# Kernel optimization log

Hardware: AMD Instinct MI355X
Metric: run time of the kernel (lower is better)

## Reference

```python
import jax, jax.numpy as jnp
import numpy as np

N = 50000
E = 400000
IN_DIM = 256
HID = 64
HEADS = 8
OUT_DIM = 40
NEG_SLOPE = 0.2  # PyG GATConv leaky-relu slope


def gat_conv(x, src, dst, W, a_src, a_dst, bias, concat):
    """One PyG-style GATConv (eval mode, self-loops already appended).
    x: [N, in], W: [in, H*C], a_src/a_dst: [H, C], bias: [H*C] or [C]."""
    H, C = a_src.shape
    h = (x @ W).reshape(N, H, C)                       # [N, H, C]
    # per-node attention logits, gathered per edge
    e_src = (h * a_src[None]).sum(-1)                  # [N, H]
    e_dst = (h * a_dst[None]).sum(-1)                  # [N, H]
    alpha = jax.nn.leaky_relu(e_src[src] + e_dst[dst], NEG_SLOPE)  # [Etot, H]
    # segment softmax over incoming edges of each dst node
    amax = jax.ops.segment_max(alpha, dst, num_segments=N)         # [N, H]
    ex = jnp.exp(alpha - amax[dst])
    denom = jax.ops.segment_sum(ex, dst, num_segments=N)           # [N, H]
    coef = ex / denom[dst]                                         # [Etot, H]
    # weighted scatter-add of neighbor features
    msg = h[src] * coef[:, :, None]                                # [Etot, H, C]
    out = jax.ops.segment_sum(msg, dst, num_segments=N)            # [N, H, C]
    out = out.reshape(N, H * C) if concat else out.mean(axis=1)
    return out + bias


def setup_inputs() -> dict:
    key = jax.random.key(0)
    ks = jax.random.split(key, 10)
    x = jax.random.normal(ks[0], (N, IN_DIM), dtype=jnp.float32)
    edge_index = jax.random.randint(ks[1], (2, E), 0, N, dtype=jnp.int32)
    g1 = 1.0 / np.sqrt(IN_DIM)
    g2 = 1.0 / np.sqrt(HID * HEADS)
    W1 = jax.random.normal(ks[2], (IN_DIM, HEADS * HID), dtype=jnp.float32) * g1
    a_src1 = jax.random.normal(ks[3], (HEADS, HID), dtype=jnp.float32) * 0.1
    a_dst1 = jax.random.normal(ks[4], (HEADS, HID), dtype=jnp.float32) * 0.1
    b1 = jnp.zeros((HEADS * HID,), dtype=jnp.float32)
    W2 = jax.random.normal(ks[5], (HEADS * HID, OUT_DIM), dtype=jnp.float32) * g2
    a_src2 = jax.random.normal(ks[6], (1, OUT_DIM), dtype=jnp.float32) * 0.1
    a_dst2 = jax.random.normal(ks[7], (1, OUT_DIM), dtype=jnp.float32) * 0.1
    b2 = jnp.zeros((OUT_DIM,), dtype=jnp.float32)
    return {"x": x, "edge_index": edge_index, "W1": W1, "a_src1": a_src1,
            "a_dst1": a_dst1, "b1": b1, "W2": W2, "a_src2": a_src2,
            "a_dst2": a_dst2, "b2": b2}


def reference(x, edge_index, W1, a_src1, a_dst1, b1, W2, a_src2, a_dst2, b2):
    # append self loops (PyG GATConv default add_self_loops=True)
    loop = jnp.arange(N, dtype=edge_index.dtype)
    src = jnp.concatenate([edge_index[0], loop])
    dst = jnp.concatenate([edge_index[1], loop])
    h = gat_conv(x, src, dst, W1, a_src1, a_dst1, b1, concat=True)
    h = jax.nn.elu(h)
    # dropout is identity in eval mode
    out = gat_conv(h, src, dst, W2, a_src2, a_dst2, b2, concat=False)
    return out
```

## Files before the change

kernel.cpp:

```cpp
#include <hip/hip_runtime.h>
#include <hip/hip_bf16.h>
#include <math.h>

#define IN_DIM 256
#define HEADS 8
#define HID 64
#define HC1 512
#define OUT_DIM 40
#define NEG_SLOPE 0.2f
#define CAP 64

typedef __attribute__((ext_vector_type(8))) short short8;
typedef __attribute__((ext_vector_type(4))) float f32x4;

__device__ __forceinline__ unsigned short f2b(float f) {
    __hip_bfloat16 h = __float2bfloat16(f);
    unsigned short u;
    __builtin_memcpy(&u, &h, 2);
    return u;
}

#define LRELU(a) ((a) > 0.f ? (a) : NEG_SLOPE * (a))

#define NB_W ((HC1 * IN_DIM + 48 * HC1 + 255) / 256)

__global__ __launch_bounds__(256) void prologue_kernel(
    const float* __restrict__ W1, const float* __restrict__ W2,
    __hip_bfloat16* __restrict__ W1T, __hip_bfloat16* __restrict__ W2T,
    const int* __restrict__ ei, int* __restrict__ cnt,
    int* __restrict__ csr_src, int E, int ET)
{
    int b = blockIdx.x;
    if (b < NB_W) {
        int i = b * 256 + threadIdx.x;
        if (i < HC1 * IN_DIM) {
            int n = i >> 8, k = i & 255;
            W1T[i] = __float2bfloat16(W1[(size_t)k * HC1 + n]);
        }
        int j = i - HC1 * IN_DIM;
        if (j >= 0 && j < 48 * HC1) {
            int n = j >> 9, k = j & 511;
            W2T[j] = __float2bfloat16(n < OUT_DIM ? W2[(size_t)k * OUT_DIM + n] : 0.f);
        }
    } else {
        int e = (b - NB_W) * 256 + threadIdx.x;
        if (e >= ET) return;
        int s, d;
        if (e < E) { s = ei[e]; d = ei[E + e]; } else { s = d = e - E; }
        int pos = atomicAdd(&cnt[d], 1);
        csr_src[((size_t)d << 6) + pos] = s;
    }
}

__global__ __launch_bounds__(512) void gemm1_mfma(
    const float* __restrict__ x, const __hip_bfloat16* __restrict__ W1T,
    const float* __restrict__ a_src1, const float* __restrict__ a_dst1,
    __hip_bfloat16* __restrict__ h1, float* __restrict__ e_src1,
    float* __restrict__ e_dst1, int N)
{
    __shared__ __hip_bfloat16 As[64][268];
    const int tid = threadIdx.x;
    const int row0 = blockIdx.x * 64;

    {
        int rr = tid >> 3;
        int cb = (tid & 7) * 32;
        int rowc = row0 + rr; if (rowc >= N) rowc = N - 1;
        const float* xp = x + (size_t)rowc * IN_DIM + cb;
#pragma unroll
        for (int j = 0; j < 4; ++j) {
            float4 a0 = *(const float4*)(xp + 8 * j);
            float4 a1 = *(const float4*)(xp + 8 * j + 4);
            short8 v;
            v[0] = f2b(a0.x); v[1] = f2b(a0.y); v[2] = f2b(a0.z); v[3] = f2b(a0.w);
            v[4] = f2b(a1.x); v[5] = f2b(a1.y); v[6] = f2b(a1.z); v[7] = f2b(a1.w);
            *(short8*)(&As[rr][cb + 8 * j]) = v;
        }
    }
    __syncthreads();

    const int w = tid >> 6;
    const int lane = tid & 63;
    const int r = lane & 15, g = lane >> 4;

    f32x4 acc[4][4] = {};
    const short* bp = (const short*)W1T + (size_t)(w * 64 + r) * IN_DIM + 8 * g;

#pragma unroll 2
    for (int kk = 0; kk < IN_DIM; kk += 32) {
        short8 af[4];
#pragma unroll
        for (int rt = 0; rt < 4; ++rt)
            af[rt] = *(const short8*)(&As[rt * 16 + r][kk + 8 * g]);
        short8 bf[4];
#pragma unroll
        for (int t = 0; t < 4; ++t)
            bf[t] = *(const short8*)(bp + (size_t)t * 16 * IN_DIM + kk);
#pragma unroll
        for (int t = 0; t < 4; ++t)
#pragma unroll
            for (int rt = 0; rt < 4; ++rt)
                acc[rt][t] = __builtin_amdgcn_mfma_f32_16x16x32_bf16(
                    af[rt], bf[t], acc[rt][t], 0, 0, 0);
    }

#pragma unroll
    for (int rt = 0; rt < 4; ++rt)
#pragma unroll
        for (int t = 0; t < 4; ++t) {
            int c = w * 64 + t * 16 + r;
#pragma unroll
            for (int q = 0; q < 4; ++q) {
                int row = row0 + rt * 16 + 4 * g + q;
                if (row < N)
                    h1[(size_t)row * HC1 + c] = __float2bfloat16(acc[rt][t][q]);
            }
        }

    float a1v[4], a2v[4];
#pragma unroll
    for (int t = 0; t < 4; ++t) {
        a1v[t] = a_src1[w * 64 + t * 16 + r];
        a2v[t] = a_dst1[w * 64 + t * 16 + r];
    }
#pragma unroll
    for (int rt = 0; rt < 4; ++rt) {
        float ps[4] = {}, pd[4] = {};
#pragma unroll
        for (int t = 0; t < 4; ++t)
#pragma unroll
            for (int q = 0; q < 4; ++q) {
                ps[q] += acc[rt][t][q] * a1v[t];
                pd[q] += acc[rt][t][q] * a2v[t];
            }
#pragma unroll
        for (int off = 1; off < 16; off <<= 1)
#pragma unroll
            for (int q = 0; q < 4; ++q) {
                ps[q] += __shfl_xor(ps[q], off);
                pd[q] += __shfl_xor(pd[q], off);
            }
        if (r == 0) {
#pragma unroll
            for (int q = 0; q < 4; ++q) {
                int row = row0 + rt * 16 + 4 * g + q;
                if (row < N) {
                    e_src1[row * 8 + w] = ps[q];
                    e_dst1[row * 8 + w] = pd[q];
                }
            }
        }
    }
}

__global__ __launch_bounds__(256) void gather1_kernel(
    const int* __restrict__ cnt, const int* __restrict__ csr_src,
    const __hip_bfloat16* __restrict__ h1, const float* __restrict__ e_src,
    const float* __restrict__ e_dst, const float* __restrict__ b1,
    __hip_bfloat16* __restrict__ hmid, int N)
{
    int d = blockIdx.x * 4 + (threadIdx.x >> 6);
    if (d >= N) return;
    const int lane = threadIdx.x & 63;
    const int h0 = lane >> 3;
    const size_t base = (size_t)d << 6;
    const int deg = cnt[d];
    const float edv = e_dst[d * 8 + (lane & 7)];

    float acc[8] = {};
    float ssum = 0.f;

    const int nch = (deg + 7) >> 3;
    for (int c = 0; c < nch; ++c) {
        int i = c * 8 + (lane >> 3);
        int ii = i < deg ? i : deg - 1;
        int s = csr_src[base + ii];
        float v = e_src[s * 8 + (lane & 7)] + edv;
        float coef = (i < deg) ? __expf(LRELU(v)) : 0.f;

        int emax = deg - c * 8; if (emax > 8) emax = 8;
        for (int e = 0; e < emax; ++e) {
            float ce = __shfl(coef, e * 8 + h0);
            int se = __shfl(s, e * 8);
            uint4 u = *(const uint4*)(h1 + ((size_t)se << 9) + 8 * lane);
            acc[0] += ce * __uint_as_float(u.x << 16);
            acc[1] += ce * __uint_as_float(u.x & 0xffff0000u);
            acc[2] += ce * __uint_as_float(u.y << 16);
            acc[3] += ce * __uint_as_float(u.y & 0xffff0000u);
            acc[4] += ce * __uint_as_float(u.z << 16);
            acc[5] += ce * __uint_as_float(u.z & 0xffff0000u);
            acc[6] += ce * __uint_as_float(u.w << 16);
            acc[7] += ce * __uint_as_float(u.w & 0xffff0000u);
            ssum += ce;
        }
    }

    float inv = 1.f / ssum;
    float4 b0 = *(const float4*)(b1 + 8 * lane);
    float4 b4 = *(const float4*)(b1 + 8 * lane + 4);
    float ob[8];
    ob[0] = acc[0] * inv + b0.x; ob[1] = acc[1] * inv + b0.y;
    ob[2] = acc[2] * inv + b0.z; ob[3] = acc[3] * inv + b0.w;
    ob[4] = acc[4] * inv + b4.x; ob[5] = acc[5] * inv + b4.y;
    ob[6] = acc[6] * inv + b4.z; ob[7] = acc[7] * inv + b4.w;
    unsigned short rr[8];
#pragma unroll
    for (int j = 0; j < 8; ++j) {
        float o = ob[j];
        o = o > 0.f ? o : expm1f(o);
        rr[j] = f2b(o);
    }
    *(uint4*)(hmid + (size_t)d * HC1 + 8 * lane) = *(uint4*)rr;
}

__global__ __launch_bounds__(256) void gemm2_mfma(
    const __hip_bfloat16* __restrict__ hmid, const __hip_bfloat16* __restrict__ W2T,
    const float* __restrict__ a_src2, const float* __restrict__ a_dst2,
    __hip_bfloat16* __restrict__ h2, float* __restrict__ e_src2,
    float* __restrict__ e_dst2, int N)
{
    __shared__ __hip_bfloat16 Bs[48][520];
    const int tid = threadIdx.x;

    {
        const short* wp = (const short*)W2T;
#pragma unroll
        for (int i = 0; i < 12; ++i) {
            int idx = tid + i * 256;
            int row = idx >> 6, ch = idx & 63;
            *(short8*)(&Bs[row][ch * 8]) = *(const short8*)(wp + (size_t)row * HC1 + ch * 8);
        }
    }
    __syncthreads();

    const int w = tid >> 6;
    const int lane = tid & 63;
    const int r = lane & 15, g = lane >> 4;
    const int rowW = blockIdx.x * 64 + w * 16;

    int arow = rowW + r; if (arow >= N) arow = N - 1;
    const short* ap = (const short*)hmid + (size_t)arow * HC1 + 8 * g;

    f32x4 acc[3] = {};
#pragma unroll 4
    for (int kk = 0; kk < HC1; kk += 32) {
        short8 af = *(const short8*)(ap + kk);
        short8 bf[3];
#pragma unroll
        for (int t = 0; t < 3; ++t)
            bf[t] = *(const short8*)(&Bs[t * 16 + r][kk + 8 * g]);
#pragma unroll
        for (int t = 0; t < 3; ++t)
            acc[t] = __builtin_amdgcn_mfma_f32_16x16x32_bf16(af, bf[t], acc[t], 0, 0, 0);
    }

#pragma unroll
    for (int t = 0; t < 3; ++t) {
        int c = t * 16 + r;
        if (c < OUT_DIM) {
#pragma unroll
            for (int q = 0; q < 4; ++q) {
                int row = rowW + 4 * g + q;
                if (row < N) h2[(size_t)row * OUT_DIM + c] = __float2bfloat16(acc[t][q]);
            }
        }
    }

    float as[3], ad[3];
#pragma unroll
    for (int t = 0; t < 3; ++t) {
        int c = t * 16 + r;
        as[t] = (c < OUT_DIM) ? a_src2[c] : 0.f;
        ad[t] = (c < OUT_DIM) ? a_dst2[c] : 0.f;
    }
    float ps[4] = {}, pd[4] = {};
#pragma unroll
    for (int t = 0; t < 3; ++t)
#pragma unroll
        for (int q = 0; q < 4; ++q) {
            ps[q] += acc[t][q] * as[t];
            pd[q] += acc[t][q] * ad[t];
        }
#pragma unroll
    for (int off = 1; off < 16; off <<= 1)
#pragma unroll
        for (int q = 0; q < 4; ++q) {
            ps[q] += __shfl_xor(ps[q], off);
            pd[q] += __shfl_xor(pd[q], off);
        }
    if (r == 0) {
#pragma unroll
        for (int q = 0; q < 4; ++q) {
            int row = rowW + 4 * g + q;
            if (row < N) { e_src2[row] = ps[q]; e_dst2[row] = pd[q]; }
        }
    }
}

__global__ __launch_bounds__(256) void gather2_kernel(
    const int* __restrict__ cnt, const int* __restrict__ csr_src,
    const __hip_bfloat16* __restrict__ h2, const float* __restrict__ e_src,
    const float* __restrict__ e_dst, const float* __restrict__ b2,
    float* __restrict__ out, int N)
{
    int wid = (blockIdx.x * blockDim.x + threadIdx.x) >> 6;
    if (wid >= N) return;
    int lane = threadIdx.x & 63;
    const size_t base = (size_t)wid << 6;
    const int end = cnt[wid];
    float ed = e_dst[wid];
    bool act = lane < OUT_DIM;
    int ln = act ? lane : 0;
    const unsigned short* h2u = (const unsigned short*)h2;

    float acc = 0.f, ssum = 0.f;
    int j = 0;
    for (; j + 4 <= end; j += 4) {
        int s0 = csr_src[base + j], s1 = csr_src[base + j + 1];
        int s2 = csr_src[base + j + 2], s3 = csr_src[base + j + 3];
        float v0 = e_src[s0] + ed, v1 = e_src[s1] + ed;
        float v2 = e_src[s2] + ed, v3 = e_src[s3] + ed;
        unsigned f0 = h2u[(size_t)s0 * OUT_DIM + ln];
        unsigned f1 = h2u[(size_t)s1 * OUT_DIM + ln];
        unsigned f2 = h2u[(size_t)s2 * OUT_DIM + ln];
        unsigned f3 = h2u[(size_t)s3 * OUT_DIM + ln];
        float e0 = __expf(LRELU(v0)), e1 = __expf(LRELU(v1));
        float e2 = __expf(LRELU(v2)), e3 = __expf(LRELU(v3));
        acc += e0 * __uint_as_float(f0 << 16) + e1 * __uint_as_float(f1 << 16)
             + e2 * __uint_as_float(f2 << 16) + e3 * __uint_as_float(f3 << 16);
        ssum += e0 + e1 + e2 + e3;
    }
    for (; j < end; ++j) {
        int s0 = csr_src[base + j];
        float v0 = e_src[s0] + ed;
        unsigned f0 = h2u[(size_t)s0 * OUT_DIM + ln];
        float e0 = __expf(LRELU(v0));
        acc += e0 * __uint_as_float(f0 << 16);
        ssum += e0;
    }
    if (act)
        out[(size_t)wid * OUT_DIM + lane] = acc / ssum + b2[lane];
}

extern "C" void kernel_launch(void* const* d_in, const int* in_sizes, int n_in,
                              void* d_out, int out_size, void* d_ws, size_t ws_size,
                              hipStream_t stream)
{
    const float* x      = (const float*)d_in[0];
    const int*   ei     = (const int*)d_in[1];
    const float* W1     = (const float*)d_in[2];
    const float* a_src1 = (const float*)d_in[3];
    const float* a_dst1 = (const float*)d_in[4];
    const float* b1     = (const float*)d_in[5];
    const float* W2     = (const float*)d_in[6];
    const float* a_src2 = (const float*)d_in[7];
    const float* a_dst2 = (const float*)d_in[8];
    const float* b2     = (const float*)d_in[9];
    float* out = (float*)d_out;

    const int N  = in_sizes[0] / IN_DIM;
    const int E  = in_sizes[1] / 2;
    const int ET = E + N;

    char* p = (char*)d_ws;
    auto alloc = [&](size_t bytes) -> void* {
        void* r = (void*)p;
        p += (bytes + 255) & ~(size_t)255;
        return r;
    };
    __hip_bfloat16* h1b    = (__hip_bfloat16*)alloc((size_t)N * HC1 * 2);
    __hip_bfloat16* hmid   = (__hip_bfloat16*)alloc((size_t)N * HC1 * 2);
    __hip_bfloat16* h2     = (__hip_bfloat16*)alloc((size_t)N * OUT_DIM * 2);
    float*    e_src1  = (float*)alloc((size_t)N * HEADS * 4);
    float*    e_dst1  = (float*)alloc((size_t)N * HEADS * 4);
    float*    e_src2  = (float*)alloc((size_t)N * 4);
    float*    e_dst2  = (float*)alloc((size_t)N * 4);
    int*      cnt     = (int*)alloc((size_t)N * 4);
    int*      csr_src = (int*)alloc((size_t)N * CAP * 4);
    __hip_bfloat16* W1T = (__hip_bfloat16*)alloc((size_t)HC1 * IN_DIM * 2);
    __hip_bfloat16* W2T = (__hip_bfloat16*)alloc((size_t)48 * HC1 * 2);

    const int nbET = (ET + 255) / 256;

    hipMemsetAsync(cnt, 0, (size_t)N * 4, stream);
    prologue_kernel<<<NB_W + nbET, 256, 0, stream>>>(W1, W2, W1T, W2T, ei,
                                                     cnt, csr_src, E, ET);

    gemm1_mfma<<<(N + 63) / 64, 512, 0, stream>>>(x, W1T, a_src1, a_dst1, h1b,
                                                  e_src1, e_dst1, N);
    gather1_kernel<<<(N + 3) / 4, 256, 0, stream>>>(cnt, csr_src, h1b, e_src1,
                                                    e_dst1, b1, hmid, N);

    gemm2_mfma<<<(N + 63) / 64, 256, 0, stream>>>(hmid, W2T, a_src2, a_dst2, h2,
                                                  e_src2, e_dst2, N);
    gather2_kernel<<<(N + 3) / 4, 256, 0, stream>>>(cnt, csr_src, h2, e_src2,
                                                    e_dst2, b2, out, N);
}
```

Before: 206.0 us.

## Retile gemm1 to 32-row blocks with 4 waves each covering two heads

Changes the first-layer GEMM tile from 64 rows by 512 columns with 8 waves to 32 rows with 4 waves, where each wave computes 128 columns (two heads) over two row tiles. This doubles the grid size and halves the block size and LDS use, aiming for better occupancy and load balance. The attention-logit reduction is restructured to handle two heads per wave. The trade-off is that each W1T fragment is reused across fewer rows, so more B-operand traffic goes to global memory or cache.

```diff
diff --git a/kernel.cpp b/kernel.cpp
--- a/kernel.cpp
+++ b/kernel.cpp
@@ -52,15 +52,15 @@
     }
 }
 
-__global__ __launch_bounds__(512) void gemm1_mfma(
+__global__ __launch_bounds__(256) void gemm1_mfma(
     const float* __restrict__ x, const __hip_bfloat16* __restrict__ W1T,
     const float* __restrict__ a_src1, const float* __restrict__ a_dst1,
     __hip_bfloat16* __restrict__ h1, float* __restrict__ e_src1,
     float* __restrict__ e_dst1, int N)
 {
-    __shared__ __hip_bfloat16 As[64][268];
+    __shared__ __hip_bfloat16 As[32][268];
     const int tid = threadIdx.x;
-    const int row0 = blockIdx.x * 64;
+    const int row0 = blockIdx.x * 32;
 
     {
         int rr = tid >> 3;
@@ -83,32 +83,32 @@
     const int lane = tid & 63;
     const int r = lane & 15, g = lane >> 4;
 
-    f32x4 acc[4][4] = {};
-    const short* bp = (const short*)W1T + (size_t)(w * 64 + r) * IN_DIM + 8 * g;
+    f32x4 acc[2][8] = {};
+    const short* bp = (const short*)W1T + (size_t)(w * 128 + r) * IN_DIM + 8 * g;
 
 #pragma unroll 2
     for (int kk = 0; kk < IN_DIM; kk += 32) {
-        short8 af[4];
-#pragma unroll
-        for (int rt = 0; rt < 4; ++rt)
+        short8 af[2];
+#pragma unroll
+        for (int rt = 0; rt < 2; ++rt)
             af[rt] = *(const short8*)(&As[rt * 16 + r][kk + 8 * g]);
-        short8 bf[4];
-#pragma unroll
-        for (int t = 0; t < 4; ++t)
+        short8 bf[8];
+#pragma unroll
+        for (int t = 0; t < 8; ++t)
             bf[t] = *(const short8*)(bp + (size_t)t * 16 * IN_DIM + kk);
 #pragma unroll
-        for (int t = 0; t < 4; ++t)
-#pragma unroll
-            for (int rt = 0; rt < 4; ++rt)
+        for (int t = 0; t < 8; ++t)
+#pragma unroll
+            for (int rt = 0; rt < 2; ++rt)
                 acc[rt][t] = __builtin_amdgcn_mfma_f32_16x16x32_bf16(
                     af[rt], bf[t], acc[rt][t], 0, 0, 0);
     }
 
 #pragma unroll
-    for (int rt = 0; rt < 4; ++rt)
-#pragma unroll
-        for (int t = 0; t < 4; ++t) {
-            int c = w * 64 + t * 16 + r;
+    for (int rt = 0; rt < 2; ++rt)
+#pragma unroll
+        for (int t = 0; t < 8; ++t) {
+            int c = w * 128 + t * 16 + r;
 #pragma unroll
             for (int q = 0; q < 4; ++q) {
                 int row = row0 + rt * 16 + 4 * g + q;
@@ -117,38 +117,43 @@
             }
         }
 
-    float a1v[4], a2v[4];
-#pragma unroll
-    for (int t = 0; t < 4; ++t) {
-        a1v[t] = a_src1[w * 64 + t * 16 + r];
-        a2v[t] = a_dst1[w * 64 + t * 16 + r];
-    }
-#pragma unroll
-    for (int rt = 0; rt < 4; ++rt) {
-        float ps[4] = {}, pd[4] = {};
-#pragma unroll
-        for (int t = 0; t < 4; ++t)
-#pragma unroll
-            for (int q = 0; q < 4; ++q) {
-                ps[q] += acc[rt][t][q] * a1v[t];
-                pd[q] += acc[rt][t][q] * a2v[t];
-            }
+#pragma unroll
+    for (int hh = 0; hh < 2; ++hh) {
+        float ps[2][4] = {}, pd[2][4] = {};
+#pragma unroll
+        for (int tt = 0; tt < 4; ++tt) {
+            int t = hh * 4 + tt;
+            int cc = (2 * w + hh) * HID + tt * 16 + r;
+            float a1v = a_src1[cc];
+            float a2v = a_dst1[cc];
+#pragma unroll
+            for (int rt = 0; rt < 2; ++rt)
+#pragma unroll
+                for (int q = 0; q < 4; ++q) {
+                    ps[rt][q] += acc[rt][t][q] * a1v;
+                    pd[rt][q] += acc[rt][t][q] * a2v;
+                }
+        }
 #pragma unroll
         for (int off = 1; off < 16; off <<= 1)
 #pragma unroll
-            for (int q = 0; q < 4; ++q) {
-                ps[q] += __shfl_xor(ps[q], off);
-                pd[q] += __shfl_xor(pd[q], off);
-            }
+            for (int rt = 0; rt < 2; ++rt)
+#pragma unroll
+                for (int q = 0; q < 4; ++q) {
+                    ps[rt][q] += __shfl_xor(ps[rt][q], off);
+                    pd[rt][q] += __shfl_xor(pd[rt][q], off);
+                }
         if (r == 0) {
 #pragma unroll
-            for (int q = 0; q < 4; ++q) {
-                int row = row0 + rt * 16 + 4 * g + q;
-                if (row < N) {
-                    e_src1[row * 8 + w] = ps[q];
-                    e_dst1[row * 8 + w] = pd[q];
+            for (int rt = 0; rt < 2; ++rt)
+#pragma unroll
+                for (int q = 0; q < 4; ++q) {
+                    int row = row0 + rt * 16 + 4 * g + q;
+                    if (row < N) {
+                        e_src1[row * 8 + 2 * w + hh] = ps[rt][q];
+                        e_dst1[row * 8 + 2 * w + hh] = pd[rt][q];
+                    }
                 }
-            }
         }
     }
 }
@@ -386,7 +391,7 @@
     prologue_kernel<<<NB_W + nbET, 256, 0, stream>>>(W1, W2, W1T, W2T, ei,
                                                      cnt, csr_src, E, ET);
 
-    gemm1_mfma<<<(N + 63) / 64, 512, 0, stream>>>(x, W1T, a_src1, a_dst1, h1b,
+    gemm1_mfma<<<(N + 31) / 32, 256, 0, stream>>>(x, W1T, a_src1, a_dst1, h1b,
                                                   e_src1, e_dst1, N);
     gather1_kernel<<<(N + 3) / 4, 256, 0, stream>>>(cnt, csr_src, h1b, e_src1,
                                                     e_dst1, b1, hmid, N);
```

After: 230.5 us. 11.9% more time.
